# Kernel optimization log

Measured on AMD Instinct MI355X. Metric: run time of the kernel, lower is better.

Reference implementation:

```python
import jax, jax.numpy as jnp
import numpy as np
import math

INPUT_SIZE = 768
OUTPUT_SIZE = 3072
INS = (8, 12, 8)     # inputs for size=768 (input_size < output_size, no swap)
OUTS = (16, 12, 16)  # outputs
# num singular values via quadratic formula from the torch code
_a = INS[2] * OUTS[2]
_b = INS[0] * OUTS[0] + INS[1] * OUTS[1]
_c = -INPUT_SIZE * OUTPUT_SIZE
NUM_S = int(((-_b + math.sqrt(_b * _b - 4 * _a * _c)) / (2 * _a)) // 1)  # = 134
N_TOKENS = 32768


def _xavier(key, shape, gain):
    # xavier_uniform over first-two-dims fan (matches torch fan computation:
    # fan_in = shape[1]*prod(shape[2:]), fan_out = shape[0]*prod(shape[2:]))
    recf = np.prod(shape[2:]).astype(np.float64) if len(shape) > 2 else 1.0
    fan_in = shape[1] * recf
    fan_out = shape[0] * recf
    bound = gain * math.sqrt(6.0 / (fan_in + fan_out))
    return jax.random.uniform(key, shape, jnp.float32, -bound, bound)


def setup_inputs() -> dict:
    key = jax.random.key(0)
    k0, k1, k2, k3 = jax.random.split(key, 4)
    g = math.sqrt(2.0)
    x = jax.random.normal(k0, (N_TOKENS, INPUT_SIZE), jnp.float32)
    W_1 = _xavier(k1, (INS[0], OUTS[0], NUM_S), g)            # (8,16,134)
    W_2 = _xavier(k2, (NUM_S, INS[1], OUTS[1], NUM_S), g)      # (134,12,12,134)
    W_3 = _xavier(k3, (NUM_S, INS[2], OUTS[2]), g)             # (134,8,16)
    b = jnp.zeros((OUTPUT_SIZE,), jnp.float32)
    return {"x": x, "W_1": W_1, "W_2": W_2, "W_3": W_3, "b": b}


def reference(x, W_1, W_2, W_3, b):
    # W[i,I,a, o,O,bb] = sum_{s,S} W_1[i,o,s] W_2[s,I,O,S] W_3[S,a,bb]
    W = jnp.einsum('ios,sIOS,Sab->iIaoOb', W_1, W_2, W_3)
    # rearrange '(i I a)(o O b)' -> row-major reshape
    W = W.reshape(INPUT_SIZE, OUTPUT_SIZE)
    return x @ W + b
```

## Files before the change

kernel.cpp:

```cpp
#include <hip/hip_runtime.h>


typedef unsigned short u16;
typedef unsigned int   u32;
typedef short s16x8 __attribute__((ext_vector_type(8)));
typedef float f32x4 __attribute__((ext_vector_type(4)));

__device__ __forceinline__ u16 f2bf(float f) {
  u32 u = __float_as_uint(f);
  u32 r = (u + 0x7FFFu + ((u >> 16) & 1u)) >> 16;
  return (u16)r;
}

__device__ __forceinline__ void gload_lds16(const void* g, void* l) {
  __builtin_amdgcn_global_load_lds(
      (const __attribute__((address_space(1))) void*)g,
      (__attribute__((address_space(3))) void*)l, 16, 0, 0);
}

__global__ __launch_bounds__(256) void xconv_kernel(const float* __restrict__ x,
                                                    u16* __restrict__ xb) {
  size_t idx = ((size_t)blockIdx.x * 256 + threadIdx.x) * 8;
  float4 v0 = *(const float4*)(x + idx);
  float4 v1 = *(const float4*)(x + idx + 4);
  uint4 o;
  o.x = (u32)f2bf(v0.x) | ((u32)f2bf(v0.y) << 16);
  o.y = (u32)f2bf(v0.z) | ((u32)f2bf(v0.w) << 16);
  o.z = (u32)f2bf(v1.x) | ((u32)f2bf(v1.y) << 16);
  o.w = (u32)f2bf(v1.z) | ((u32)f2bf(v1.w) << 16);
  *(uint4*)(xb + idx) = o;
}

__global__ __launch_bounds__(256) void a1_kernel(const float* __restrict__ W1,
                                                 const float* __restrict__ W2,
                                                 float* __restrict__ T1) {
  __shared__ float lW1[32 * 136];
  const int t = threadIdx.x;
  const int iog = blockIdx.y;
  const int ios = blockIdx.x * 256 + t;
  for (int idx = t; idx < 32 * 136; idx += 256) {
    int u = idx / 136, s = idx - u * 136;
    lW1[idx] = (s < 134) ? W1[(size_t)(iog * 32 + u) * 134 + s] : 0.f;
  }
  __syncthreads();
  const bool valid = ios < 19296;
  float acc[32];
#pragma unroll
  for (int u = 0; u < 32; u++) acc[u] = 0.f;
  for (int s4 = 0; s4 < 136; s4 += 4) {
    float wa = (valid && s4 + 0 < 134) ? W2[(size_t)(s4 + 0) * 19296 + ios] : 0.f;
    float wb = (valid && s4 + 1 < 134) ? W2[(size_t)(s4 + 1) * 19296 + ios] : 0.f;
    float wc = (valid && s4 + 2 < 134) ? W2[(size_t)(s4 + 2) * 19296 + ios] : 0.f;
    float wd = (valid && s4 + 3 < 134) ? W2[(size_t)(s4 + 3) * 19296 + ios] : 0.f;
#pragma unroll
    for (int u = 0; u < 32; u++) {
      float4 wv = *(const float4*)&lW1[u * 136 + s4];
      acc[u] += wv.x * wa + wv.y * wb + wv.z * wc + wv.w * wd;
    }
  }
  if (valid) {
#pragma unroll
    for (int u = 0; u < 32; u++)
      T1[(size_t)(iog * 32 + u) * 19296 + ios] = acc[u];
  }
}

__global__ __launch_bounds__(128) void a2_kernel(const float* __restrict__ T1,
                                                 const float* __restrict__ W3,
                                                 u16* __restrict__ Wt) {
  __shared__ float lT[12 * 136];
  __shared__ u16 lOut[192 * 8];
  const int t = threadIdx.x;
  const int io = blockIdx.x;
  const int I = blockIdx.y;
  const int i = io >> 4, o = io & 15;
  const float* src = T1 + (size_t)io * 19296 + (size_t)I * 1608;
  for (int idx = t; idx < 12 * 136; idx += 128) {
    int O = idx / 136, S = idx - O * 136;
    lT[idx] = (S < 134) ? src[O * 134 + S] : 0.f;
  }
  __syncthreads();
  float acc[12];
#pragma unroll
  for (int O = 0; O < 12; O++) acc[O] = 0.f;
  for (int S4 = 0; S4 < 136; S4 += 4) {
    float w0 = (S4 + 0 < 134) ? W3[(S4 + 0) * 128 + t] : 0.f;
    float w1 = (S4 + 1 < 134) ? W3[(S4 + 1) * 128 + t] : 0.f;
    float w2 = (S4 + 2 < 134) ? W3[(S4 + 2) * 128 + t] : 0.f;
    float w3 = (S4 + 3 < 134) ? W3[(S4 + 3) * 128 + t] : 0.f;
#pragma unroll
    for (int O = 0; O < 12; O++) {
      float4 tv = *(const float4*)&lT[O * 136 + S4];
      acc[O] += tv.x * w0 + tv.y * w1 + tv.z * w2 + tv.w * w3;
    }
  }
  const int a = t >> 4, b = t & 15;
#pragma unroll
  for (int O = 0; O < 12; O++) lOut[(O * 16 + b) * 8 + a] = f2bf(acc[O]);
  __syncthreads();
  for (int rr = t; rr < 192; rr += 128) {
    int col = o * 192 + rr;
    *(uint4*)&Wt[(size_t)col * 768 + i * 96 + I * 8] = *(const uint4*)&lOut[rr * 8];
  }
}

__global__ __launch_bounds__(256) void gemm_kernel(const u16* __restrict__ A,
                                                   const u16* __restrict__ Bt,
                                                   const float* __restrict__ bias,
                                                   float* __restrict__ C) {
  __shared__ u16 lA[128 * 32];
  __shared__ u16 lB[128 * 32];
  const int t = threadIdx.x;
  const int wave = t >> 6, lane = t & 63;
  const int q = lane >> 4, l16 = lane & 15;
  const int wr = wave >> 1, wc = wave & 1;
  const int blockN = blockIdx.x * 128, blockM = blockIdx.y * 128;

  f32x4 acc[4][4];
  const f32x4 z = {0.f, 0.f, 0.f, 0.f};
#pragma unroll
  for (int mi = 0; mi < 4; mi++)
#pragma unroll
    for (int ni = 0; ni < 4; ni++) acc[mi][ni] = z;

  const int rowA = t >> 2;
  const int kc = (t & 3) * 8;
  const u16* gA = A + (size_t)(blockM + rowA) * 768 + kc;
  const u16* gB = Bt + (size_t)(blockN + rowA) * 768 + kc;
  u16* lAw0 = lA + wave * 512;
  u16* lAw1 = lA + 2048 + wave * 512;
  u16* lBw0 = lB + wave * 512;
  u16* lBw1 = lB + 2048 + wave * 512;

  for (int kt = 0; kt < 24; ++kt) {
    const int k0 = kt * 32;
    gload_lds16(gA + k0, lAw0);
    gload_lds16(gA + 64 * 768 + k0, lAw1);
    gload_lds16(gB + k0, lBw0);
    gload_lds16(gB + 64 * 768 + k0, lBw1);
    __syncthreads();
    s16x8 af[4], bf[4];
#pragma unroll
    for (int mi = 0; mi < 4; mi++)
      af[mi] = *(const s16x8*)&lA[(wr * 64 + mi * 16 + l16) * 32 + q * 8];
#pragma unroll
    for (int ni = 0; ni < 4; ni++)
      bf[ni] = *(const s16x8*)&lB[(wc * 64 + ni * 16 + l16) * 32 + q * 8];
#pragma unroll
    for (int mi = 0; mi < 4; mi++)
#pragma unroll
      for (int ni = 0; ni < 4; ni++)
        acc[mi][ni] = __builtin_amdgcn_mfma_f32_16x16x32_bf16(af[mi], bf[ni], acc[mi][ni], 0, 0, 0);
    __syncthreads();
  }

#pragma unroll
  for (int ni = 0; ni < 4; ni++) {
    const int col = blockN + wc * 64 + ni * 16 + l16;
    const float bv = bias[col];
#pragma unroll
    for (int mi = 0; mi < 4; mi++) {
      const int row = blockM + wr * 64 + mi * 16 + q * 4;
      float* cp = C + (size_t)row * 3072 + col;
      cp[0]        = acc[mi][ni][0] + bv;
      cp[3072]     = acc[mi][ni][1] + bv;
      cp[2 * 3072] = acc[mi][ni][2] + bv;
      cp[3 * 3072] = acc[mi][ni][3] + bv;
    }
  }
}

extern "C" void kernel_launch(void* const* d_in, const int* in_sizes, int n_in,
                              void* d_out, int out_size, void* d_ws, size_t ws_size,
                              hipStream_t stream) {
  const float* x  = (const float*)d_in[0];
  const float* W1 = (const float*)d_in[1];
  const float* W2 = (const float*)d_in[2];
  const float* W3 = (const float*)d_in[3];
  const float* b  = (const float*)d_in[4];
  float* out = (float*)d_out;

  char* ws = (char*)d_ws;
  u16* Xb   = (u16*)ws;
  u16* Wt   = (u16*)(ws + 50331648);
  float* T1 = (float*)(ws + 50331648 + 4718592);

  xconv_kernel<<<12288, 256, 0, stream>>>(x, Xb);
  a1_kernel<<<dim3(76, 4), 256, 0, stream>>>(W1, W2, T1);
  a2_kernel<<<dim3(128, 12), 128, 0, stream>>>(T1, W3, Wt);
  gemm_kernel<<<dim3(24, 256), 256, 0, stream>>>(Xb, Wt, b, out);
}
```

Baseline: 727.6 us.

## Rewrite GEMM with 256x256 tiles, 4-stage LDS pipeline, swizzled LDS and block order

The bf16 GEMM moves from 128x128 tiles with a single LDS buffer and two barriers per k-step to 256x256 tiles, 512 threads and a 4-deep ring of LDS buffers filled by direct global-to-LDS loads. Explicit vmcnt waits let loads for later k-steps run while the current one computes. The LDS k-offset is XOR-swizzled to cut bank conflicts, and the 1D grid is remapped so neighbouring blocks share tiles in L2. It adds register pressure (128 accumulator floats per thread) and 128KB of LDS per block, which may limit occupancy.

```diff
diff --git a/kernel.cpp b/kernel.cpp
--- a/kernel.cpp
+++ b/kernel.cpp
@@ -104,63 +104,126 @@
   }
 }
 
-__global__ __launch_bounds__(256) void gemm_kernel(const u16* __restrict__ A,
-                                                   const u16* __restrict__ Bt,
-                                                   const float* __restrict__ bias,
-                                                   float* __restrict__ C) {
-  __shared__ u16 lA[128 * 32];
-  __shared__ u16 lB[128 * 32];
+
+template <int N>
+__device__ __forceinline__ void vmcnt_wait() {
+  if constexpr (N == 12)     asm volatile("s_waitcnt vmcnt(12)" ::: "memory");
+  else if constexpr (N == 8) asm volatile("s_waitcnt vmcnt(8)"  ::: "memory");
+  else if constexpr (N == 4) asm volatile("s_waitcnt vmcnt(4)"  ::: "memory");
+  else                       asm volatile("s_waitcnt vmcnt(0)"  ::: "memory");
+}
+
+__global__ __launch_bounds__(512, 2) void gemm_kernel(const u16* __restrict__ A,
+                                                      const u16* __restrict__ Bt,
+                                                      const float* __restrict__ bias,
+                                                      float* __restrict__ C) {
+  __shared__ u16 smem[4 * 16384];
   const int t = threadIdx.x;
-  const int wave = t >> 6, lane = t & 63;
+  const int lane = t & 63, wid = t >> 6;
+  const int wr = wid >> 2, wc = wid & 3;
   const int q = lane >> 4, l16 = lane & 15;
-  const int wr = wave >> 1, wc = wave & 1;
-  const int blockN = blockIdx.x * 128, blockM = blockIdx.y * 128;
-
-  f32x4 acc[4][4];
+
+  const int bid = blockIdx.x;
+  const int swz = (bid & 7) * 192 + (bid >> 3);
+  const int nIdx = swz % 12, mIdx = swz / 12;
+  const int blockM = mIdx * 256, blockN = nIdx * 256;
+
+  const int kb_src = (((t & 3) ^ ((t >> 3) & 3)) << 4);
+  const int rA = t >> 2;
+  const u16* gAs = A  + (size_t)(blockM + rA) * 768 + (kb_src >> 1);
+  const u16* gBs = Bt + (size_t)(blockN + rA) * 768 + (kb_src >> 1);
+
+#define STAGE(b_, kt_) do {                                     \
+    const u16* ga_ = gAs + (kt_) * 32;                          \
+    const u16* gb_ = gBs + (kt_) * 32;                          \
+    u16* lw_ = &smem[(b_) * 16384 + wid * 512];                 \
+    gload_lds16(ga_,             lw_);                          \
+    gload_lds16(ga_ + 128 * 768, lw_ + 4096);                   \
+    gload_lds16(gb_,             lw_ + 8192);                   \
+    gload_lds16(gb_ + 128 * 768, lw_ + 12288);                  \
+  } while (0)
+
+  f32x4 acc[8][4];
   const f32x4 z = {0.f, 0.f, 0.f, 0.f};
 #pragma unroll
-  for (int mi = 0; mi < 4; mi++)
+  for (int mi = 0; mi < 8; mi++)
 #pragma unroll
     for (int ni = 0; ni < 4; ni++) acc[mi][ni] = z;
 
-  const int rowA = t >> 2;
-  const int kc = (t & 3) * 8;
-  const u16* gA = A + (size_t)(blockM + rowA) * 768 + kc;
-  const u16* gB = Bt + (size_t)(blockN + rowA) * 768 + kc;
-  u16* lAw0 = lA + wave * 512;
-  u16* lAw1 = lA + 2048 + wave * 512;
-  u16* lBw0 = lB + wave * 512;
-  u16* lBw1 = lB + 2048 + wave * 512;
-
-  for (int kt = 0; kt < 24; ++kt) {
-    const int k0 = kt * 32;
-    gload_lds16(gA + k0, lAw0);
-    gload_lds16(gA + 64 * 768 + k0, lAw1);
-    gload_lds16(gB + k0, lBw0);
-    gload_lds16(gB + 64 * 768 + k0, lBw1);
-    __syncthreads();
-    s16x8 af[4], bf[4];
-#pragma unroll
-    for (int mi = 0; mi < 4; mi++)
-      af[mi] = *(const s16x8*)&lA[(wr * 64 + mi * 16 + l16) * 32 + q * 8];
-#pragma unroll
-    for (int ni = 0; ni < 4; ni++)
-      bf[ni] = *(const s16x8*)&lB[(wc * 64 + ni * 16 + l16) * 32 + q * 8];
-#pragma unroll
-    for (int mi = 0; mi < 4; mi++)
-#pragma unroll
-      for (int ni = 0; ni < 4; ni++)
-        acc[mi][ni] = __builtin_amdgcn_mfma_f32_16x16x32_bf16(af[mi], bf[ni], acc[mi][ni], 0, 0, 0);
-    __syncthreads();
-  }
-
+  const int koff = (q << 3) ^ (((l16 >> 1) & 3) << 3);
+  const int aRow = wr * 128 + l16;
+  const int bRow = wc * 64 + l16;
+
+#define COMPUTE(bb_) do {                                                       \
+    const u16* lA_ = &smem[(bb_) * 16384];                                      \
+    const u16* lB_ = lA_ + 8192;                                                \
+    s16x8 bg[4], af[4], af2[4];                                                 \
+    _Pragma("unroll")                                                           \
+    for (int ni = 0; ni < 4; ni++)                                              \
+      bg[ni] = *(const s16x8*)&lB_[(bRow + ni * 16) * 32 + koff];               \
+    _Pragma("unroll")                                                           \
+    for (int mi = 0; mi < 4; mi++)                                              \
+      af[mi] = *(const s16x8*)&lA_[(aRow + mi * 16) * 32 + koff];               \
+    _Pragma("unroll")                                                           \
+    for (int mi = 0; mi < 4; mi++)                                              \
+      af2[mi] = *(const s16x8*)&lA_[(aRow + (mi + 4) * 16) * 32 + koff];        \
+    __builtin_amdgcn_s_setprio(1);                                              \
+    _Pragma("unroll")                                                           \
+    for (int mi = 0; mi < 4; mi++)                                              \
+      _Pragma("unroll")                                                         \
+      for (int ni = 0; ni < 4; ni++)                                            \
+        acc[mi][ni] = __builtin_amdgcn_mfma_f32_16x16x32_bf16(af[mi], bg[ni],   \
+                                                              acc[mi][ni], 0, 0, 0); \
+    __builtin_amdgcn_s_setprio(0);                                              \
+    __builtin_amdgcn_s_setprio(1);                                              \
+    _Pragma("unroll")                                                           \
+    for (int mi = 0; mi < 4; mi++)                                              \
+      _Pragma("unroll")                                                         \
+      for (int ni = 0; ni < 4; ni++)                                            \
+        acc[mi + 4][ni] = __builtin_amdgcn_mfma_f32_16x16x32_bf16(af2[mi], bg[ni], \
+                                                              acc[mi + 4][ni], 0, 0, 0); \
+    __builtin_amdgcn_s_setprio(0);                                              \
+  } while (0)
+
+  STAGE(0, 0);
+  STAGE(1, 1);
+  STAGE(2, 2);
+
+  for (int tt = 0; tt < 21; ++tt) {
+    STAGE((tt + 3) & 3, tt + 3);
+    vmcnt_wait<12>();
+    __builtin_amdgcn_s_barrier();
+    __builtin_amdgcn_sched_barrier(0);
+    COMPUTE(tt & 3);
+    __builtin_amdgcn_sched_barrier(0);
+    __builtin_amdgcn_s_barrier();
+    __builtin_amdgcn_sched_barrier(0);
+  }
+  vmcnt_wait<8>();
+  __builtin_amdgcn_s_barrier();
+  __builtin_amdgcn_sched_barrier(0);
+  COMPUTE(1);
+  __builtin_amdgcn_sched_barrier(0);
+  __builtin_amdgcn_s_barrier();
+  vmcnt_wait<4>();
+  __builtin_amdgcn_s_barrier();
+  __builtin_amdgcn_sched_barrier(0);
+  COMPUTE(2);
+  __builtin_amdgcn_sched_barrier(0);
+  __builtin_amdgcn_s_barrier();
+  vmcnt_wait<0>();
+  __builtin_amdgcn_s_barrier();
+  __builtin_amdgcn_sched_barrier(0);
+  COMPUTE(3);
+
+  const int colBase = blockN + wc * 64 + l16;
 #pragma unroll
   for (int ni = 0; ni < 4; ni++) {
-    const int col = blockN + wc * 64 + ni * 16 + l16;
+    const int col = colBase + ni * 16;
     const float bv = bias[col];
 #pragma unroll
-    for (int mi = 0; mi < 4; mi++) {
-      const int row = blockM + wr * 64 + mi * 16 + q * 4;
+    for (int mi = 0; mi < 8; mi++) {
+      const int row = blockM + wr * 128 + mi * 16 + q * 4;
       float* cp = C + (size_t)row * 3072 + col;
       cp[0]        = acc[mi][ni][0] + bv;
       cp[3072]     = acc[mi][ni][1] + bv;
@@ -168,6 +231,8 @@
       cp[3 * 3072] = acc[mi][ni][3] + bv;
     }
   }
+#undef STAGE
+#undef COMPUTE
 }
 
 extern "C" void kernel_launch(void* const* d_in, const int* in_sizes, int n_in,
@@ -188,5 +253,5 @@
   xconv_kernel<<<12288, 256, 0, stream>>>(x, Xb);
   a1_kernel<<<dim3(76, 4), 256, 0, stream>>>(W1, W2, T1);
   a2_kernel<<<dim3(128, 12), 128, 0, stream>>>(T1, W3, Wt);
-  gemm_kernel<<<dim3(24, 256), 256, 0, stream>>>(Xb, Wt, b, out);
-}
+  gemm_kernel<<<dim3(1536), 512, 0, stream>>>(Xb, Wt, b, out);
+}
```

Measured after the change: 712.2 us. 2.1% less time.
